# Optimization experiments

Measured on AMD Instinct MI355X. Metric: run time of the kernel, lower is better.

## Reference

```python
import jax, jax.numpy as jnp
import numpy as np

BN = 128  # weight block rows
BK = 128  # quantization block along K
FP8_MAX = 448.0  # float8_e4m3fn max finite value
F8 = jnp.float8_e4m3fn


def _quant_dequant_act(x):
    # Dynamic per-token, per-128-block FP8 quantization (scale = amax/448), then dequant.
    M, K = x.shape
    xb = x.reshape(M, K // BK, BK)
    amax = jnp.max(jnp.abs(xb), axis=-1, keepdims=True)
    scale = jnp.maximum(amax, 1e-12) / FP8_MAX
    q = jnp.clip(xb / scale, -FP8_MAX, FP8_MAX).astype(F8)
    return (q.astype(jnp.float32) * scale).reshape(M, K)


def _dequant_weight(w, s):
    # w: (N, K) fp8, s: (N//BN, K//BK) f32 block scales
    N, K = w.shape
    sf = jnp.repeat(jnp.repeat(s, BN, axis=0), BK, axis=1)[:N, :K]
    return w.astype(jnp.float32) * sf


def _fp8_linear(x, w, s):
    # y = dequant(quant(x)) @ dequant(w)^T  -- matches w8a8_fp8_matmul semantics
    return _quant_dequant_act(x) @ _dequant_weight(w, s).T


def _quantize_weight(key, shape):
    E, N, K = shape
    w = jax.random.normal(key, shape, jnp.float32) * 0.02
    wb = w.reshape(E, N // BN, BN, K // BK, BK)
    amax = jnp.max(jnp.abs(wb), axis=(2, 4), keepdims=True)
    scale = jnp.maximum(amax, 1e-12) / FP8_MAX
    q = jnp.clip(wb / scale, -FP8_MAX, FP8_MAX).astype(F8).reshape(E, N, K)
    return q, scale.reshape(E, N // BN, K // BK)


def setup_inputs() -> dict:
    key = jax.random.key(0)
    k1, k2, k3, k4, k5 = jax.random.split(key, 5)
    T, H, I, E, TOPK = 2048, 2048, 1408, 8, 2
    hidden_states = jax.random.normal(k1, (T, H), jnp.float32)
    top_k_index = jax.random.randint(k2, (T, TOPK), 0, E).astype(jnp.int64)
    w = jax.random.uniform(k3, (T, TOPK), jnp.float32)
    top_k_weights = w / jnp.sum(w, axis=-1, keepdims=True)
    gate_up_proj, gate_up_proj_scale_inv = _quantize_weight(k4, (E, 2 * I, H))
    down_proj, down_proj_scale_inv = _quantize_weight(k5, (E, H, I))
    return {
        "hidden_states": hidden_states,
        "top_k_index": top_k_index,
        "top_k_weights": top_k_weights,
        "gate_up_proj": gate_up_proj,
        "gate_up_proj_scale_inv": gate_up_proj_scale_inv,
        "down_proj": down_proj,
        "down_proj_scale_inv": down_proj_scale_inv,
    }


def reference(hidden_states, top_k_index, top_k_weights, gate_up_proj,
              gate_up_proj_scale_inv, down_proj, down_proj_scale_inv):
    E = gate_up_proj.shape[0]
    I = down_proj.shape[-1]
    # Activation quantization is per-token: identical for every expert, compute once.
    x_dq = _quant_dequant_act(hidden_states)  # (T, H)
    out = jnp.zeros_like(hidden_states, dtype=jnp.float32)
    for e in range(E):  # fixed small expert loop (structural, not data dim)
        gu = x_dq @ _dequant_weight(gate_up_proj[e], gate_up_proj_scale_inv[e]).T  # (T, 2I)
        gate, up = gu[:, :I], gu[:, I:]
        h = jax.nn.silu(gate) * up
        d = _fp8_linear(h, down_proj[e], down_proj_scale_inv[e])  # (T, H)
        # routing weight for this expert per token (sums duplicates like index_add_)
        rw = jnp.sum(jnp.where(top_k_index == e, top_k_weights, 0.0), axis=-1)  # (T,)
        out = out + rw[:, None] * d
    return out.astype(hidden_states.dtype)
```

## Files before the change

kernel.cpp:

```cpp
#include <hip/hip_runtime.h>
#include <cstdint>
#include <cstddef>

using f32x4 = __attribute__((ext_vector_type(4))) float;

#define TDIM 2048
#define HDIM 2048
#define IDIM 1408
#define NEXP 8
#define NKB1 16
#define NNB1 11
#define NKB2 11
#define MAXM 4096
#define LDA 144

__device__ __forceinline__ f32x4 mfma_fp8(long a, long b, f32x4 c) {
  return __builtin_amdgcn_mfma_f32_16x16x32_fp8_fp8(a, b, c, 0, 0, 0);
}

__device__ __forceinline__ uint32_t f8_1(float q) {
  q = fminf(fmaxf(q, -448.f), 448.f);
  return (uint32_t)__builtin_amdgcn_cvt_pk_fp8_f32(q, q, 0, false) & 0xffu;
}

__device__ __forceinline__ float bf16_to_f32(uint32_t bits16) {
  union { uint32_t u; float f; } c;
  c.u = bits16 << 16;
  return c.f;
}

__global__ void zero_kernel(float* __restrict__ out, int* __restrict__ cnt) {
  const int i = blockIdx.x * 256 + threadIdx.x;
  ((f32x4*)out)[i] = f32x4{0.f, 0.f, 0.f, 0.f};
  if (blockIdx.x == 0 && threadIdx.x < 8) cnt[threadIdx.x] = 0;
}

__global__ void sniff_kernel(const uint16_t* __restrict__ a,
                             const uint16_t* __restrict__ b,
                             int* __restrict__ modes) {
  if (threadIdx.x == 0 && blockIdx.x == 0) {
    unsigned acc = 0;
    for (int i = 0; i < 128; ++i) acc |= a[2 * i];
    modes[0] = (acc == 0) ? 1 : 0;
    acc = 0;
    for (int i = 0; i < 128; ++i) acc |= b[2 * i];
    modes[1] = (acc == 0) ? 1 : 0;
  }
}

__global__ void repack_kernel(const void* __restrict__ in, uint8_t* __restrict__ out,
                              int n8, const int* __restrict__ modes, int midx) {
  const int i = blockIdx.x * 256 + threadIdx.x;
  if (i >= n8) return;
  const int m = modes[midx];
  float f[8];
  if (m == 1) {
    const float4* p = (const float4*)in;
    float4 a = p[2 * i], b = p[2 * i + 1];
    f[0] = a.x; f[1] = a.y; f[2] = a.z; f[3] = a.w;
    f[4] = b.x; f[5] = b.y; f[6] = b.z; f[7] = b.w;
  } else {
    uint4 v = ((const uint4*)in)[i];
#pragma unroll
    for (int j = 0; j < 4; ++j) {
      uint32_t w = (&v.x)[j];
      f[2 * j]     = bf16_to_f32(w & 0xffffu);
      f[2 * j + 1] = bf16_to_f32(w >> 16);
    }
  }
  uint32_t lo = 0, hi = 0;
#pragma unroll
  for (int j = 0; j < 8; ++j) {
    uint32_t b8 = f8_1(f[j]);
    if (j < 4) lo |= b8 << (8 * j);
    else       hi |= b8 << (8 * (j - 4));
  }
  ((uint2*)out)[i] = make_uint2(lo, hi);
}

__global__ void quantx_kernel(const float* __restrict__ x,
                              uint8_t* __restrict__ xq, float* __restrict__ xs) {
  const int gid = blockIdx.x * 4 + (threadIdx.x >> 6);
  const int lane = threadIdx.x & 63;
  const int r = gid >> 4, kb = gid & 15;
  const float2 v = *(const float2*)(x + (size_t)r * HDIM + kb * 128 + lane * 2);
  float a = fmaxf(fabsf(v.x), fabsf(v.y));
#pragma unroll
  for (int d = 1; d < 64; d <<= 1) a = fmaxf(a, __shfl_xor(a, d));
  const float s = fmaxf(a, 1e-12f) / 448.f;
  const uint32_t b0 = f8_1(v.x / s);
  const uint32_t b1 = f8_1(v.y / s);
  *(uint16_t*)(xq + (size_t)r * HDIM + kb * 128 + lane * 2) = (uint16_t)(b0 | (b1 << 8));
  if (lane == 0) xs[r * 16 + kb] = s;
}

__global__ void route_kernel(const void* __restrict__ idxraw,
                             int* __restrict__ list, int* __restrict__ cnt) {
  const long long* p = (const long long*)idxraw;
  unsigned hi = 0;
#pragma unroll
  for (int j = 0; j < 16; ++j) hi |= (unsigned)((unsigned long long)p[j] >> 32);
  const int i = blockIdx.x * 256 + threadIdx.x;
  int e;
  if (hi == 0) {
    e = (int)p[i];
  } else {
    long long v = p[i >> 1];
    e = (int)((i & 1) ? (v >> 32) : (v & 0xffffffffLL));
  }
  e &= 7;
  const int pos = atomicAdd(&cnt[e], 1);
  list[e * MAXM + pos] = i;
}

__global__ __launch_bounds__(512) void gemm1_kernel(
    const uint8_t* __restrict__ xq, const float* __restrict__ xs,
    const uint8_t* __restrict__ w, const float* __restrict__ wscl,
    const int* __restrict__ list, const int* __restrict__ cnt,
    uint8_t* __restrict__ hq, float* __restrict__ hs) {
  const int e = blockIdx.z, mt = blockIdx.y, nb = blockIdx.x;
  const int M = cnt[e];
  if (mt * 128 >= M) return;
  __shared__ __align__(16) uint8_t As[128 * LDA];
  __shared__ __align__(16) uint8_t Bg[128 * LDA];
  __shared__ __align__(16) uint8_t Bu[128 * LDA];
  __shared__ int slots[128];
  __shared__ __align__(16) float sxs[128];
  __shared__ __align__(16) float amx[512];
  const int tid = threadIdx.x, lane = tid & 63, wid = tid >> 6;
  const int wr = wid >> 2, wc = wid & 3;
  if (tid < 128) {
    int m = mt * 128 + tid;
    slots[tid] = list[e * MAXM + (m < M ? m : 0)];
  }
  __syncthreads();
  const int srow = tid >> 3;
  const int cj = (tid & 7) << 4;
  const long tokA0 = slots[srow] >> 1;
  const long tokA1 = slots[srow + 64] >> 1;
  const int my_tok = (tid < 128) ? (slots[tid] >> 1) : 0;
  const uint8_t* pA0 = xq + tokA0 * HDIM + cj;
  const uint8_t* pA1 = xq + tokA1 * HDIM + cj;
  const size_t wb = (size_t)e * (2 * IDIM) * HDIM;
  const uint8_t* pG0 = w + wb + (size_t)(nb * 128 + srow) * HDIM + cj;
  const uint8_t* pU0 = w + wb + (size_t)(IDIM + nb * 128 + srow) * HDIM + cj;
  const float* wsg = wscl + (size_t)e * 352 + nb * 16;
  const float* wsu = wsg + 176;
  const float* pSX = xs + (size_t)my_tok * 16;
  f32x4 accg[4][2] = {};
  f32x4 accu[4][2] = {};
  const int kbyte = (lane >> 4) << 3;
  f32x4 ra0, ra1, rg0, rg1, ru0, ru1;
  float rs;
  ra0 = *(const f32x4*)(pA0);
  ra1 = *(const f32x4*)(pA1);
  rg0 = *(const f32x4*)(pG0);
  rg1 = *(const f32x4*)(pG0 + 64 * HDIM);
  ru0 = *(const f32x4*)(pU0);
  ru1 = *(const f32x4*)(pU0 + 64 * HDIM);
  rs = (tid < 128) ? pSX[0] : 0.f;
  for (int kb = 0; kb < NKB1; ++kb) {
    __syncthreads();
    *(f32x4*)(As + srow * LDA + cj) = ra0;
    *(f32x4*)(As + (srow + 64) * LDA + cj) = ra1;
    *(f32x4*)(Bg + srow * LDA + cj) = rg0;
    *(f32x4*)(Bg + (srow + 64) * LDA + cj) = rg1;
    *(f32x4*)(Bu + srow * LDA + cj) = ru0;
    *(f32x4*)(Bu + (srow + 64) * LDA + cj) = ru1;
    if (tid < 128) sxs[tid] = rs;
    __syncthreads();
    if (kb + 1 < NKB1) {
      const int ko = (kb + 1) << 7;
      ra0 = *(const f32x4*)(pA0 + ko);
      ra1 = *(const f32x4*)(pA1 + ko);
      rg0 = *(const f32x4*)(pG0 + ko);
      rg1 = *(const f32x4*)(pG0 + 64 * HDIM + ko);
      ru0 = *(const f32x4*)(pU0 + ko);
      ru1 = *(const f32x4*)(pU0 + 64 * HDIM + ko);
      rs = (tid < 128) ? pSX[kb + 1] : 0.f;
    }
    const float swg = wsg[kb];
    const float swu = wsu[kb];
    long af[4][4], bgf[2][4], buf_[2][4];
#pragma unroll
    for (int mi = 0; mi < 4; ++mi) {
      const int r = wr * 64 + mi * 16 + (lane & 15);
      const uint8_t* bp = As + r * LDA;
#pragma unroll
      for (int kc = 0; kc < 4; ++kc)
        af[mi][kc] = *(const long*)(bp + (kc << 5) + kbyte);
    }
#pragma unroll
    for (int ni = 0; ni < 2; ++ni) {
      const int r = wc * 32 + ni * 16 + (lane & 15);
      const uint8_t* bpg = Bg + r * LDA;
      const uint8_t* bpu = Bu + r * LDA;
#pragma unroll
      for (int kc = 0; kc < 4; ++kc) {
        bgf[ni][kc] = *(const long*)(bpg + (kc << 5) + kbyte);
        buf_[ni][kc] = *(const long*)(bpu + (kc << 5) + kbyte);
      }
    }
    f32x4 sx[4];
#pragma unroll
    for (int mi = 0; mi < 4; ++mi)
      sx[mi] = *(const f32x4*)(sxs + wr * 64 + mi * 16 + ((lane >> 4) << 2));
#pragma unroll
    for (int mi = 0; mi < 4; ++mi)
#pragma unroll
      for (int ni = 0; ni < 2; ++ni) {
        f32x4 pg = {0.f, 0.f, 0.f, 0.f};
        f32x4 pu = {0.f, 0.f, 0.f, 0.f};
#pragma unroll
        for (int kc = 0; kc < 4; ++kc) {
          pg = mfma_fp8(af[mi][kc], bgf[ni][kc], pg);
          pu = mfma_fp8(af[mi][kc], buf_[ni][kc], pu);
        }
#pragma unroll
        for (int j = 0; j < 4; ++j) {
          accg[mi][ni][j] += pg[j] * (sx[mi][j] * swg);
          accu[mi][ni][j] += pu[j] * (sx[mi][j] * swu);
        }
      }
  }
  f32x4 hv[4][2];
  f32x4 rmax[4];
#pragma unroll
  for (int mi = 0; mi < 4; ++mi) {
#pragma unroll
    for (int ni = 0; ni < 2; ++ni)
#pragma unroll
      for (int j = 0; j < 4; ++j) {
        float g = accg[mi][ni][j];
        float u = accu[mi][ni][j];
        float h = (g / (1.f + expf(-g))) * u;
        hv[mi][ni][j] = h;
        float ah = fabsf(h);
        rmax[mi][j] = (ni == 0) ? ah : fmaxf(rmax[mi][j], ah);
      }
#pragma unroll
    for (int d = 1; d < 16; d <<= 1)
#pragma unroll
      for (int j = 0; j < 4; ++j)
        rmax[mi][j] = fmaxf(rmax[mi][j], __shfl_xor(rmax[mi][j], d));
  }
  __syncthreads();
  if ((lane & 15) == 0) {
#pragma unroll
    for (int mi = 0; mi < 4; ++mi)
#pragma unroll
      for (int j = 0; j < 4; ++j) {
        int row = wr * 64 + mi * 16 + ((lane >> 4) << 2) + j;
        amx[row * 4 + wc] = rmax[mi][j];
      }
  }
  __syncthreads();
  const int Mrem = M - mt * 128;
#pragma unroll
  for (int mi = 0; mi < 4; ++mi)
#pragma unroll
    for (int j = 0; j < 4; ++j) {
      const int row = wr * 64 + mi * 16 + ((lane >> 4) << 2) + j;
      f32x4 a4 = *(const f32x4*)(amx + row * 4);
      float am = fmaxf(fmaxf(a4[0], a4[1]), fmaxf(a4[2], a4[3]));
      float s = fmaxf(am, 1e-12f) / 448.f;
      if (row < Mrem) {
        const int slot = slots[row];
        uint8_t* hp = hq + (size_t)slot * IDIM + nb * 128 + wc * 32 + (lane & 15);
        hp[0]  = (uint8_t)f8_1(hv[mi][0][j] / s);
        hp[16] = (uint8_t)f8_1(hv[mi][1][j] / s);
        if (wc == 0 && (lane & 15) == 0) hs[slot * 11 + nb] = s;
      }
    }
}

__global__ __launch_bounds__(512) void gemm2_kernel(
    const uint8_t* __restrict__ hq, const float* __restrict__ hs,
    const uint8_t* __restrict__ w, const float* __restrict__ wscl,
    const int* __restrict__ list, const int* __restrict__ cnt,
    const float* __restrict__ tkw, float* __restrict__ out) {
  const int e = blockIdx.z, mt = blockIdx.y, nt = blockIdx.x;
  const int M = cnt[e];
  if (mt * 128 >= M) return;
  __shared__ __align__(16) uint8_t As[128 * LDA];
  __shared__ __align__(16) uint8_t Bs[256 * LDA];
  __shared__ int slots[128];
  __shared__ float rwl[128];
  __shared__ __align__(16) float sxs[128];
  const int tid = threadIdx.x, lane = tid & 63, wid = tid >> 6;
  const int wr = wid >> 2, wc = wid & 3;
  if (tid < 128) {
    int m = mt * 128 + tid;
    int slot = list[e * MAXM + (m < M ? m : 0)];
    slots[tid] = slot;
    rwl[tid] = (m < M) ? tkw[slot] : 0.f;
  }
  __syncthreads();
  const int srow = tid >> 3;
  const int cj = (tid & 7) << 4;
  const long slotA0 = slots[srow];
  const long slotA1 = slots[srow + 64];
  const int my_slot = (tid < 128) ? slots[tid] : 0;
  const uint8_t* pA0 = hq + slotA0 * IDIM + cj;
  const uint8_t* pA1 = hq + slotA1 * IDIM + cj;
  const uint8_t* pB = w + (size_t)e * HDIM * IDIM + (size_t)(nt * 256 + srow) * IDIM + cj;
  const float* wsd = wscl + (size_t)e * 176 + (nt * 2 + (wc >> 1)) * 11;
  const float* pSX = hs + (size_t)my_slot * 11;
  f32x4 acc[4][4] = {};
  const int kbyte = (lane >> 4) << 3;
  f32x4 ra0, ra1, rb0, rb1, rb2, rb3;
  float rs;
  ra0 = *(const f32x4*)(pA0);
  ra1 = *(const f32x4*)(pA1);
  rb0 = *(const f32x4*)(pB);
  rb1 = *(const f32x4*)(pB + (size_t)64 * IDIM);
  rb2 = *(const f32x4*)(pB + (size_t)128 * IDIM);
  rb3 = *(const f32x4*)(pB + (size_t)192 * IDIM);
  rs = (tid < 128) ? pSX[0] : 0.f;
  for (int kb = 0; kb < NKB2; ++kb) {
    __syncthreads();
    *(f32x4*)(As + srow * LDA + cj) = ra0;
    *(f32x4*)(As + (srow + 64) * LDA + cj) = ra1;
    *(f32x4*)(Bs + srow * LDA + cj) = rb0;
    *(f32x4*)(Bs + (srow + 64) * LDA + cj) = rb1;
    *(f32x4*)(Bs + (srow + 128) * LDA + cj) = rb2;
    *(f32x4*)(Bs + (srow + 192) * LDA + cj) = rb3;
    if (tid < 128) sxs[tid] = rs;
    __syncthreads();
    if (kb + 1 < NKB2) {
      const int ko = (kb + 1) << 7;
      ra0 = *(const f32x4*)(pA0 + ko);
      ra1 = *(const f32x4*)(pA1 + ko);
      rb0 = *(const f32x4*)(pB + ko);
      rb1 = *(const f32x4*)(pB + (size_t)64 * IDIM + ko);
      rb2 = *(const f32x4*)(pB + (size_t)128 * IDIM + ko);
      rb3 = *(const f32x4*)(pB + (size_t)192 * IDIM + ko);
      rs = (tid < 128) ? pSX[kb + 1] : 0.f;
    }
    const float swd = wsd[kb];
    long af[4][4], bf[4][4];
#pragma unroll
    for (int mi = 0; mi < 4; ++mi) {
      const int r = wr * 64 + mi * 16 + (lane & 15);
      const uint8_t* bp = As + r * LDA;
#pragma unroll
      for (int kc = 0; kc < 4; ++kc)
        af[mi][kc] = *(const long*)(bp + (kc << 5) + kbyte);
    }
#pragma unroll
    for (int ni = 0; ni < 4; ++ni) {
      const int r = wc * 64 + ni * 16 + (lane & 15);
      const uint8_t* bp = Bs + r * LDA;
#pragma unroll
      for (int kc = 0; kc < 4; ++kc)
        bf[ni][kc] = *(const long*)(bp + (kc << 5) + kbyte);
    }
    f32x4 sx[4];
#pragma unroll
    for (int mi = 0; mi < 4; ++mi)
      sx[mi] = *(const f32x4*)(sxs + wr * 64 + mi * 16 + ((lane >> 4) << 2));
#pragma unroll
    for (int mi = 0; mi < 4; ++mi)
#pragma unroll
      for (int ni = 0; ni < 4; ++ni) {
        f32x4 p = {0.f, 0.f, 0.f, 0.f};
#pragma unroll
        for (int kc = 0; kc < 4; ++kc) p = mfma_fp8(af[mi][kc], bf[ni][kc], p);
#pragma unroll
        for (int j = 0; j < 4; ++j) acc[mi][ni][j] += p[j] * (sx[mi][j] * swd);
      }
  }
  const int Mrem = M - mt * 128;
#pragma unroll
  for (int mi = 0; mi < 4; ++mi)
#pragma unroll
    for (int j = 0; j < 4; ++j) {
      const int row = wr * 64 + mi * 16 + ((lane >> 4) << 2) + j;
      if (row < Mrem) {
        const int slot = slots[row];
        const float rw = rwl[row];
        float* op = out + (size_t)(slot >> 1) * HDIM + nt * 256 + wc * 64 + (lane & 15);
#pragma unroll
        for (int ni = 0; ni < 4; ++ni) atomicAdd(op + ni * 16, rw * acc[mi][ni][j]);
      }
    }
}

extern "C" void kernel_launch(void* const* d_in, const int* in_sizes, int n_in,
                              void* d_out, int out_size, void* d_ws, size_t ws_size,
                              hipStream_t stream) {
  const float* hidden = (const float*)d_in[0];
  const void* topk_idx = d_in[1];
  const float* topk_w = (const float*)d_in[2];
  const void* gup_raw = d_in[3];
  const float* gup_s = (const float*)d_in[4];
  const void* dwn_raw = d_in[5];
  const float* dwn_s = (const float*)d_in[6];
  float* out = (float*)d_out;
  uint8_t* ws = (uint8_t*)d_ws;
  uint8_t* xq = ws;
  float* xs = (float*)(ws + 4194304);
  uint8_t* hq = ws + 4325376;
  float* hs = (float*)(ws + 10092544);
  int* list = (int*)(ws + 10272768);
  int* cnt = (int*)(ws + 10403840);
  int* modes = (int*)(ws + 10403904);
  uint8_t* gq = ws + 10403968;
  uint8_t* dq = ws + 56541312;
  (void)in_sizes; (void)n_in; (void)ws_size;

  zero_kernel<<<4096, 256, 0, stream>>>(out, cnt);
  sniff_kernel<<<1, 64, 0, stream>>>((const uint16_t*)gup_raw, (const uint16_t*)dwn_raw, modes);
  repack_kernel<<<(5767168 + 255) / 256, 256, 0, stream>>>(gup_raw, gq, 5767168, modes, 0);
  repack_kernel<<<(2883584 + 255) / 256, 256, 0, stream>>>(dwn_raw, dq, 2883584, modes, 1);
  quantx_kernel<<<8192, 256, 0, stream>>>(hidden, xq, xs);
  route_kernel<<<16, 256, 0, stream>>>(topk_idx, list, cnt);
  gemm1_kernel<<<dim3(NNB1, MAXM / 128, NEXP), 512, 0, stream>>>(xq, xs, gq, gup_s, list, cnt, hq, hs);
  gemm2_kernel<<<dim3(HDIM / 256, MAXM / 128, NEXP), 512, 0, stream>>>(hq, hs, dq, dwn_s, list, cnt, topk_w, out);
}
```

Measured before the change: 260.3 us.

## Load GEMM tiles directly into LDS with global_load_lds and XOR-swizzled layout

Both GEMM kernels now copy A and B tiles from global memory straight into shared memory using the global_load_lds builtin, instead of staging them through registers. The padded LDA=144 row stride is replaced by a dense 128-byte stride with an XOR swizzle on 16-byte chunks to avoid bank conflicts. This cuts register pressure and VGPR-to-LDS store instructions. The register prefetch of the next K block is gone, so global load latency is no longer overlapped with the MFMA work of the previous block, and the loop now depends on the barrier waiting for the direct-to-LDS loads.

```diff
diff --git a/kernel.cpp b/kernel.cpp
--- a/kernel.cpp
+++ b/kernel.cpp
@@ -12,7 +12,13 @@
 #define NNB1 11
 #define NKB2 11
 #define MAXM 4096
-#define LDA 144
+
+__device__ __forceinline__ void gll16(const void* g, void* l) {
+  __builtin_amdgcn_global_load_lds(
+      (__attribute__((address_space(1))) void*)(uintptr_t)g,
+      (__attribute__((address_space(3))) void*)(uint32_t)(uintptr_t)l,
+      16, 0, 0);
+}
 
 __device__ __forceinline__ f32x4 mfma_fp8(long a, long b, f32x4 c) {
   return __builtin_amdgcn_mfma_f32_16x16x32_fp8_fp8(a, b, c, 0, 0, 0);
@@ -121,9 +127,9 @@
   const int e = blockIdx.z, mt = blockIdx.y, nb = blockIdx.x;
   const int M = cnt[e];
   if (mt * 128 >= M) return;
-  __shared__ __align__(16) uint8_t As[128 * LDA];
-  __shared__ __align__(16) uint8_t Bg[128 * LDA];
-  __shared__ __align__(16) uint8_t Bu[128 * LDA];
+  __shared__ __align__(16) uint8_t As[16384];
+  __shared__ __align__(16) uint8_t Bg[16384];
+  __shared__ __align__(16) uint8_t Bu[16384];
   __shared__ int slots[128];
   __shared__ __align__(16) float sxs[128];
   __shared__ __align__(16) float amx[512];
@@ -135,70 +141,56 @@
   }
   __syncthreads();
   const int srow = tid >> 3;
-  const int cj = (tid & 7) << 4;
+  const int cj0 = ((tid & 7) ^ (srow & 7)) << 4;
   const long tokA0 = slots[srow] >> 1;
   const long tokA1 = slots[srow + 64] >> 1;
   const int my_tok = (tid < 128) ? (slots[tid] >> 1) : 0;
-  const uint8_t* pA0 = xq + tokA0 * HDIM + cj;
-  const uint8_t* pA1 = xq + tokA1 * HDIM + cj;
+  const uint8_t* pA0 = xq + tokA0 * HDIM + cj0;
+  const uint8_t* pA1 = xq + tokA1 * HDIM + cj0;
   const size_t wb = (size_t)e * (2 * IDIM) * HDIM;
-  const uint8_t* pG0 = w + wb + (size_t)(nb * 128 + srow) * HDIM + cj;
-  const uint8_t* pU0 = w + wb + (size_t)(IDIM + nb * 128 + srow) * HDIM + cj;
+  const uint8_t* pG0 = w + wb + (size_t)(nb * 128 + srow) * HDIM + cj0;
+  const uint8_t* pU0 = w + wb + (size_t)(IDIM + nb * 128 + srow) * HDIM + cj0;
   const float* wsg = wscl + (size_t)e * 352 + nb * 16;
   const float* wsu = wsg + 176;
   const float* pSX = xs + (size_t)my_tok * 16;
   f32x4 accg[4][2] = {};
   f32x4 accu[4][2] = {};
   const int kbyte = (lane >> 4) << 3;
-  f32x4 ra0, ra1, rg0, rg1, ru0, ru1;
-  float rs;
-  ra0 = *(const f32x4*)(pA0);
-  ra1 = *(const f32x4*)(pA1);
-  rg0 = *(const f32x4*)(pG0);
-  rg1 = *(const f32x4*)(pG0 + 64 * HDIM);
-  ru0 = *(const f32x4*)(pU0);
-  ru1 = *(const f32x4*)(pU0 + 64 * HDIM);
-  rs = (tid < 128) ? pSX[0] : 0.f;
+  float rs = (tid < 128) ? pSX[0] : 0.f;
   for (int kb = 0; kb < NKB1; ++kb) {
     __syncthreads();
-    *(f32x4*)(As + srow * LDA + cj) = ra0;
-    *(f32x4*)(As + (srow + 64) * LDA + cj) = ra1;
-    *(f32x4*)(Bg + srow * LDA + cj) = rg0;
-    *(f32x4*)(Bg + (srow + 64) * LDA + cj) = rg1;
-    *(f32x4*)(Bu + srow * LDA + cj) = ru0;
-    *(f32x4*)(Bu + (srow + 64) * LDA + cj) = ru1;
+    const int ko = kb << 7;
+    gll16(pA0 + ko, As + tid * 16);
+    gll16(pA1 + ko, As + 8192 + tid * 16);
+    gll16(pG0 + ko, Bg + tid * 16);
+    gll16(pG0 + 64 * HDIM + ko, Bg + 8192 + tid * 16);
+    gll16(pU0 + ko, Bu + tid * 16);
+    gll16(pU0 + 64 * HDIM + ko, Bu + 8192 + tid * 16);
     if (tid < 128) sxs[tid] = rs;
     __syncthreads();
-    if (kb + 1 < NKB1) {
-      const int ko = (kb + 1) << 7;
-      ra0 = *(const f32x4*)(pA0 + ko);
-      ra1 = *(const f32x4*)(pA1 + ko);
-      rg0 = *(const f32x4*)(pG0 + ko);
-      rg1 = *(const f32x4*)(pG0 + 64 * HDIM + ko);
-      ru0 = *(const f32x4*)(pU0 + ko);
-      ru1 = *(const f32x4*)(pU0 + 64 * HDIM + ko);
-      rs = (tid < 128) ? pSX[kb + 1] : 0.f;
-    }
+    if (kb + 1 < NKB1) rs = (tid < 128) ? pSX[kb + 1] : 0.f;
     const float swg = wsg[kb];
     const float swu = wsu[kb];
     long af[4][4], bgf[2][4], buf_[2][4];
 #pragma unroll
     for (int mi = 0; mi < 4; ++mi) {
       const int r = wr * 64 + mi * 16 + (lane & 15);
-      const uint8_t* bp = As + r * LDA;
+      const int xr = (r & 7) << 4;
+      const uint8_t* bp = As + r * 128;
 #pragma unroll
       for (int kc = 0; kc < 4; ++kc)
-        af[mi][kc] = *(const long*)(bp + (kc << 5) + kbyte);
+        af[mi][kc] = *(const long*)(bp + (((kc << 5) + kbyte) ^ xr));
     }
 #pragma unroll
     for (int ni = 0; ni < 2; ++ni) {
       const int r = wc * 32 + ni * 16 + (lane & 15);
-      const uint8_t* bpg = Bg + r * LDA;
-      const uint8_t* bpu = Bu + r * LDA;
+      const int xr = (r & 7) << 4;
+      const uint8_t* bpg = Bg + r * 128;
+      const uint8_t* bpu = Bu + r * 128;
 #pragma unroll
       for (int kc = 0; kc < 4; ++kc) {
-        bgf[ni][kc] = *(const long*)(bpg + (kc << 5) + kbyte);
-        buf_[ni][kc] = *(const long*)(bpu + (kc << 5) + kbyte);
+        bgf[ni][kc] = *(const long*)(bpg + (((kc << 5) + kbyte) ^ xr));
+        buf_[ni][kc] = *(const long*)(bpu + (((kc << 5) + kbyte) ^ xr));
       }
     }
     f32x4 sx[4];
@@ -282,8 +274,8 @@
   const int e = blockIdx.z, mt = blockIdx.y, nt = blockIdx.x;
   const int M = cnt[e];
   if (mt * 128 >= M) return;
-  __shared__ __align__(16) uint8_t As[128 * LDA];
-  __shared__ __align__(16) uint8_t Bs[256 * LDA];
+  __shared__ __align__(16) uint8_t As[16384];
+  __shared__ __align__(16) uint8_t Bs[32768];
   __shared__ int slots[128];
   __shared__ float rwl[128];
   __shared__ __align__(16) float sxs[128];
@@ -297,63 +289,48 @@
   }
   __syncthreads();
   const int srow = tid >> 3;
-  const int cj = (tid & 7) << 4;
+  const int cj0 = ((tid & 7) ^ (srow & 7)) << 4;
   const long slotA0 = slots[srow];
   const long slotA1 = slots[srow + 64];
   const int my_slot = (tid < 128) ? slots[tid] : 0;
-  const uint8_t* pA0 = hq + slotA0 * IDIM + cj;
-  const uint8_t* pA1 = hq + slotA1 * IDIM + cj;
-  const uint8_t* pB = w + (size_t)e * HDIM * IDIM + (size_t)(nt * 256 + srow) * IDIM + cj;
+  const uint8_t* pA0 = hq + slotA0 * IDIM + cj0;
+  const uint8_t* pA1 = hq + slotA1 * IDIM + cj0;
+  const uint8_t* pB = w + (size_t)e * HDIM * IDIM + (size_t)(nt * 256 + srow) * IDIM + cj0;
   const float* wsd = wscl + (size_t)e * 176 + (nt * 2 + (wc >> 1)) * 11;
   const float* pSX = hs + (size_t)my_slot * 11;
   f32x4 acc[4][4] = {};
   const int kbyte = (lane >> 4) << 3;
-  f32x4 ra0, ra1, rb0, rb1, rb2, rb3;
-  float rs;
-  ra0 = *(const f32x4*)(pA0);
-  ra1 = *(const f32x4*)(pA1);
-  rb0 = *(const f32x4*)(pB);
-  rb1 = *(const f32x4*)(pB + (size_t)64 * IDIM);
-  rb2 = *(const f32x4*)(pB + (size_t)128 * IDIM);
-  rb3 = *(const f32x4*)(pB + (size_t)192 * IDIM);
-  rs = (tid < 128) ? pSX[0] : 0.f;
+  float rs = (tid < 128) ? pSX[0] : 0.f;
   for (int kb = 0; kb < NKB2; ++kb) {
     __syncthreads();
-    *(f32x4*)(As + srow * LDA + cj) = ra0;
-    *(f32x4*)(As + (srow + 64) * LDA + cj) = ra1;
-    *(f32x4*)(Bs + srow * LDA + cj) = rb0;
-    *(f32x4*)(Bs + (srow + 64) * LDA + cj) = rb1;
-    *(f32x4*)(Bs + (srow + 128) * LDA + cj) = rb2;
-    *(f32x4*)(Bs + (srow + 192) * LDA + cj) = rb3;
+    const int ko = kb << 7;
+    gll16(pA0 + ko, As + tid * 16);
+    gll16(pA1 + ko, As + 8192 + tid * 16);
+#pragma unroll
+    for (int it = 0; it < 4; ++it)
+      gll16(pB + (size_t)(it * 64) * IDIM + ko, Bs + it * 8192 + tid * 16);
     if (tid < 128) sxs[tid] = rs;
     __syncthreads();
-    if (kb + 1 < NKB2) {
-      const int ko = (kb + 1) << 7;
-      ra0 = *(const f32x4*)(pA0 + ko);
-      ra1 = *(const f32x4*)(pA1 + ko);
-      rb0 = *(const f32x4*)(pB + ko);
-      rb1 = *(const f32x4*)(pB + (size_t)64 * IDIM + ko);
-      rb2 = *(const f32x4*)(pB + (size_t)128 * IDIM + ko);
-      rb3 = *(const f32x4*)(pB + (size_t)192 * IDIM + ko);
-      rs = (tid < 128) ? pSX[kb + 1] : 0.f;
-    }
+    if (kb + 1 < NKB2) rs = (tid < 128) ? pSX[kb + 1] : 0.f;
     const float swd = wsd[kb];
     long af[4][4], bf[4][4];
 #pragma unroll
     for (int mi = 0; mi < 4; ++mi) {
       const int r = wr * 64 + mi * 16 + (lane & 15);
-      const uint8_t* bp = As + r * LDA;
+      const int xr = (r & 7) << 4;
+      const uint8_t* bp = As + r * 128;
 #pragma unroll
       for (int kc = 0; kc < 4; ++kc)
-        af[mi][kc] = *(const long*)(bp + (kc << 5) + kbyte);
+        af[mi][kc] = *(const long*)(bp + (((kc << 5) + kbyte) ^ xr));
     }
 #pragma unroll
     for (int ni = 0; ni < 4; ++ni) {
       const int r = wc * 64 + ni * 16 + (lane & 15);
-      const uint8_t* bp = Bs + r * LDA;
+      const int xr = (r & 7) << 4;
+      const uint8_t* bp = Bs + r * 128;
 #pragma unroll
       for (int kc = 0; kc < 4; ++kc)
-        bf[ni][kc] = *(const long*)(bp + (kc << 5) + kbyte);
+        bf[ni][kc] = *(const long*)(bp + (((kc << 5) + kbyte) ^ xr));
     }
     f32x4 sx[4];
 #pragma unroll
```

After: 280.6 us. 1.08x slower.
